# Optimization experiments

Hardware: AMD Instinct MI355X
Metric: run time of the kernel (lower is better)

Reference implementation:

```python
import jax, jax.numpy as jnp
from jax import lax
import numpy as np

BIG = jnp.float32(1e6)  # 'no feature in this column' sentinel distance


def setup_inputs() -> dict:
    key = jax.random.key(0)
    k1, k2 = jax.random.split(key)
    # Binary segmentation masks in {0,1}; surf() only uses astype(bool), i.e. != 0.
    pred = (jax.random.uniform(k1, (512, 512)) > 0.5).astype(jnp.float32)
    gt = (jax.random.uniform(k2, (512, 512)) > 0.5).astype(jnp.float32)
    return {"pred": pred, "gt": gt}


def _erode(x):
    # scipy binary_erosion with connectivity-1 (cross) structure, border_value=0:
    # pixel survives iff it and its 4 neighbors are all True (out-of-bounds = False).
    p = jnp.pad(x, 1, constant_values=False)
    return x & p[:-2, 1:-1] & p[2:, 1:-1] & p[1:-1, :-2] & p[1:-1, 2:]


def _edt(feat):
    # Exact Euclidean distance from every pixel to the nearest True pixel of `feat`.
    # Equals scipy distance_transform_edt(~feat) in the original code.
    H, W = feat.shape
    # --- pass 1: per-column 1D distance |r - k| to nearest feature (two sweeps) ---
    def sweep(carry, row):
        c = jnp.where(row, jnp.float32(0.0), carry + jnp.float32(1.0))
        return c, c
    init = jnp.full((W,), BIG, dtype=jnp.float32)
    _, df = lax.scan(sweep, init, feat)          # distance to nearest feature above
    _, db = lax.scan(sweep, init, feat[::-1])    # ... below
    g = jnp.minimum(df, db[::-1])                # [H, W] vertical distance
    g2 = g * g
    # --- pass 2: row-wise min-plus over column offsets (exact, separable) ---
    j = jnp.arange(W, dtype=jnp.float32)
    delta2 = (j[:, None] - j[None, :]) ** 2      # [W(c), W(j)]
    # D[r, c] = min_j ( g2[r, j] + (c - j)^2 )   -> [H, W, W] intermediate
    d2 = jnp.min(g2[:, None, :] + delta2[None, :, :], axis=-1)
    return jnp.sqrt(d2)


def reference(pred, gt):
    p = pred != 0
    g = gt != 0
    # Surface = mask minus its erosion
    S = p & ~_erode(p)
    Sprime = g & ~_erode(g)
    dta = _edt(S)       # distance field to pred surface (== edt(~S))
    dtb = _edt(Sprime)  # distance field to gt surface
    sm = S.astype(jnp.float32)
    spm = Sprime.astype(jnp.float32)
    # mean of concat(dta[Sprime], dtb[S]) without dynamic shapes
    num = jnp.sum(dta * spm) + jnp.sum(dtb * sm)
    den = jnp.sum(spm) + jnp.sum(sm)
    return num / den
```

## Files before the change

### kernel.cpp

```cpp
#include <hip/hip_runtime.h>

#define HH 512
#define WW 512
#define NB HH

__device__ unsigned int g_ticket = 0;

#define AT_LD(p)    __hip_atomic_load((p),       __ATOMIC_RELAXED, __HIP_MEMORY_SCOPE_AGENT)
#define AT_ST(p, v) __hip_atomic_store((p), (v), __ATOMIC_RELAXED, __HIP_MEMORY_SCOPE_AGENT)
#define AT_ADD(p)   __hip_atomic_fetch_add((p), 1u, __ATOMIC_RELAXED, __HIP_MEMORY_SCOPE_AGENT)

__device__ __forceinline__ unsigned int surf2(const float* __restrict__ pa,
                                              const float* __restrict__ pb,
                                              int ru, int c) {
    const int base = ru * WW + c;
    float a_c = pa[base];
    float b_c = pb[base];
    float a_u = (ru > 0)      ? pa[base - WW] : 0.0f;
    float b_u = (ru > 0)      ? pb[base - WW] : 0.0f;
    float a_d = (ru < HH - 1) ? pa[base + WW] : 0.0f;
    float b_d = (ru < HH - 1) ? pb[base + WW] : 0.0f;
    float a_l = (c > 0)       ? pa[base - 1]  : 0.0f;
    float b_l = (c > 0)       ? pb[base - 1]  : 0.0f;
    float a_r = (c < WW - 1)  ? pa[base + 1]  : 0.0f;
    float b_r = (c < WW - 1)  ? pb[base + 1]  : 0.0f;
    unsigned int bits = 0u;
    if (a_c != 0.0f && !(a_u != 0.0f && a_d != 0.0f && a_l != 0.0f && a_r != 0.0f)) bits |= 1u;
    if (b_c != 0.0f && !(b_u != 0.0f && b_d != 0.0f && b_l != 0.0f && b_r != 0.0f)) bits |= 2u;
    return bits;
}

__global__ __launch_bounds__(512) void fused_kernel(
        const float* __restrict__ pred, const float* __restrict__ gt,
        double* __restrict__ partials, float* __restrict__ out) {
    __shared__ float2 s2[WW];
    __shared__ double lred[16];
    __shared__ int    winner;
    const int r = blockIdx.x;
    const int c = threadIdx.x;

    unsigned int own = surf2(pred, gt, r, c);
    bool fa = (own & 1u) != 0u;
    bool fb = (own & 2u) != 0u;
    int foundA = fa ? 0 : -1;
    int foundB = fb ? 0 : -1;
    for (int k = 1; k < HH && (foundA < 0 || foundB < 0); ++k) {
        int ru = r - k, rd = r + k;
        if (ru < 0 && rd >= HH) break;
        unsigned int hit = 0u;
        if (ru >= 0) hit |= surf2(pred, gt, ru, c);
        if (rd < HH) hit |= surf2(pred, gt, rd, c);
        if (foundA < 0 && (hit & 1u)) foundA = k;
        if (foundB < 0 && (hit & 2u)) foundB = k;
    }
    float sent = 1e6f + (float)((r + 1 < HH - r) ? (r + 1) : (HH - r));
    float ga = (foundA >= 0) ? (float)foundA : sent;
    float gb = (foundB >= 0) ? (float)foundB : sent;
    s2[c] = make_float2(ga * ga, gb * gb);
    __syncthreads();

    float2 o2 = s2[c];
    float besta = o2.x, bestb = o2.y;
    for (int kb = 1; kb < WW; kb += 4) {
        float kk2 = (float)(kb * kb);
        if (kk2 >= besta && kk2 >= bestb) break;
        #pragma unroll
        for (int i = 0; i < 4; ++i) {
            int k = kb + i;
            float k2 = (float)(k * k);
            int cl = c - k, cr = c + k;
            if (cl >= 0) {
                float2 g = s2[cl];
                besta = fminf(besta, g.x + k2);
                bestb = fminf(bestb, g.y + k2);
            }
            if (cr < WW) {
                float2 g = s2[cr];
                besta = fminf(besta, g.x + k2);
                bestb = fminf(bestb, g.y + k2);
            }
        }
    }

    float wA = fa ? 1.0f : 0.0f;
    float wB = fb ? 1.0f : 0.0f;
    double lnum = (double)(sqrtf(besta) * wB + sqrtf(bestb) * wA);
    double lden = (double)(wA + wB);
    for (int off = 32; off > 0; off >>= 1) {
        lnum += __shfl_down(lnum, off, 64);
        lden += __shfl_down(lden, off, 64);
    }
    int wv = c >> 6;
    if ((c & 63) == 0) { lred[wv] = lnum; lred[8 + wv] = lden; }
    __syncthreads();
    if (c == 0) {
        double n = 0.0, d = 0.0;
        #pragma unroll
        for (int i = 0; i < 8; ++i) { n += lred[i]; d += lred[8 + i]; }
        AT_ST(&partials[2 * r],     n);
        AT_ST(&partials[2 * r + 1], d);
        asm volatile("s_waitcnt vmcnt(0) lgkmcnt(0)" ::: "memory");
        unsigned int old = AT_ADD(&g_ticket);
        winner = (old == NB - 1u) ? 1 : 0;
    }
    __syncthreads();

    if (winner) {
        double n = AT_LD(&partials[2 * c]);
        double d = AT_LD(&partials[2 * c + 1]);
        for (int off = 32; off > 0; off >>= 1) {
            n += __shfl_down(n, off, 64);
            d += __shfl_down(d, off, 64);
        }
        if ((c & 63) == 0) { lred[c >> 6] = n; lred[8 + (c >> 6)] = d; }
        __syncthreads();
        if (c == 0) {
            double nn = 0.0, dd = 0.0;
            #pragma unroll
            for (int i = 0; i < 8; ++i) { nn += lred[i]; dd += lred[8 + i]; }
            out[0] = (float)(nn / dd);
            AT_ST(&g_ticket, 0u);
        }
    }
}

extern "C" void kernel_launch(void* const* d_in, const int* in_sizes, int n_in,
                              void* d_out, int out_size, void* d_ws, size_t ws_size,
                              hipStream_t stream) {
    const float* pred = (const float*)d_in[0];
    const float* gt   = (const float*)d_in[1];
    float* out = (float*)d_out;

    double* partials = (double*)d_ws;

    fused_kernel<<<dim3(NB), dim3(WW), 0, stream>>>(pred, gt, partials, out);
}
```

Measured before the change: 79.39 us.

## Stage mask rows in shared memory ring buffers for vertical surface search

```diff
diff --git a/kernel.cpp b/kernel.cpp
--- a/kernel.cpp
+++ b/kernel.cpp
@@ -10,49 +10,69 @@
 #define AT_ST(p, v) __hip_atomic_store((p), (v), __ATOMIC_RELAXED, __HIP_MEMORY_SCOPE_AGENT)
 #define AT_ADD(p)   __hip_atomic_fetch_add((p), 1u, __ATOMIC_RELAXED, __HIP_MEMORY_SCOPE_AGENT)
 
-__device__ __forceinline__ unsigned int surf2(const float* __restrict__ pa,
-                                              const float* __restrict__ pb,
-                                              int ru, int c) {
-    const int base = ru * WW + c;
-    float a_c = pa[base];
-    float b_c = pb[base];
-    float a_u = (ru > 0)      ? pa[base - WW] : 0.0f;
-    float b_u = (ru > 0)      ? pb[base - WW] : 0.0f;
-    float a_d = (ru < HH - 1) ? pa[base + WW] : 0.0f;
-    float b_d = (ru < HH - 1) ? pb[base + WW] : 0.0f;
-    float a_l = (c > 0)       ? pa[base - 1]  : 0.0f;
-    float b_l = (c > 0)       ? pb[base - 1]  : 0.0f;
-    float a_r = (c < WW - 1)  ? pa[base + 1]  : 0.0f;
-    float b_r = (c < WW - 1)  ? pb[base + 1]  : 0.0f;
-    unsigned int bits = 0u;
-    if (a_c != 0.0f && !(a_u != 0.0f && a_d != 0.0f && a_l != 0.0f && a_r != 0.0f)) bits |= 1u;
-    if (b_c != 0.0f && !(b_u != 0.0f && b_d != 0.0f && b_l != 0.0f && b_r != 0.0f)) bits |= 2u;
-    return bits;
-}
-
 __global__ __launch_bounds__(512) void fused_kernel(
         const float* __restrict__ pred, const float* __restrict__ gt,
         double* __restrict__ partials, float* __restrict__ out) {
+    __shared__ unsigned int uR[3][WW + 2];
+    __shared__ unsigned int dR[3][WW + 2];
     __shared__ float2 s2[WW];
     __shared__ double lred[16];
     __shared__ int    winner;
     const int r = blockIdx.x;
     const int c = threadIdx.x;
 
-    unsigned int own = surf2(pred, gt, r, c);
+    if (c < 6) {
+        int s = c >> 1;
+        int p = (c & 1) ? (WW + 1) : 0;
+        uR[s][p] = 0u;
+        dR[s][p] = 0u;
+    }
+
+    auto mbits = [&](int row) -> unsigned int {
+        unsigned int b = 0u;
+        if (row >= 0 && row < HH) {
+            if (pred[row * WW + c] != 0.0f) b |= 1u;
+            if (gt[row * WW + c]   != 0.0f) b |= 2u;
+        }
+        return b;
+    };
+
+    unsigned int b0 = mbits(r);
+    uR[0][c + 1] = b0;
+    dR[0][c + 1] = b0;
+    uR[1][c + 1] = mbits(r - 1);
+    dR[1][c + 1] = mbits(r + 1);
+    __syncthreads();
+
+    unsigned int own = uR[0][c + 1] &
+        ~(uR[1][c + 1] & dR[1][c + 1] & uR[0][c] & uR[0][c + 2]);
     bool fa = (own & 1u) != 0u;
     bool fb = (own & 2u) != 0u;
     int foundA = fa ? 0 : -1;
     int foundB = fb ? 0 : -1;
-    for (int k = 1; k < HH && (foundA < 0 || foundB < 0); ++k) {
-        int ru = r - k, rd = r + k;
-        if (ru < 0 && rd >= HH) break;
+    bool done = (foundA >= 0) && (foundB >= 0);
+
+    for (int k = 1; k < HH; ++k) {
+        if (__syncthreads_and((int)done)) break;
+        const int sl = (k + 1) % 3;
+        uR[sl][c + 1] = mbits(r - k - 1);
+        dR[sl][c + 1] = mbits(r + k + 1);
+        __syncthreads();
         unsigned int hit = 0u;
-        if (ru >= 0) hit |= surf2(pred, gt, ru, c);
-        if (rd < HH) hit |= surf2(pred, gt, rd, c);
+        const int km = k % 3, kp = (k - 1 + 3) % 3;
+        if (r - k >= 0) {
+            hit |= uR[km][c + 1] &
+                ~(uR[sl][c + 1] & uR[kp][c + 1] & uR[km][c] & uR[km][c + 2]);
+        }
+        if (r + k < HH) {
+            hit |= dR[km][c + 1] &
+                ~(dR[sl][c + 1] & dR[kp][c + 1] & dR[km][c] & dR[km][c + 2]);
+        }
         if (foundA < 0 && (hit & 1u)) foundA = k;
         if (foundB < 0 && (hit & 2u)) foundB = k;
+        done = (foundA >= 0) && (foundB >= 0);
     }
+
     float sent = 1e6f + (float)((r + 1 < HH - r) ? (r + 1) : (HH - r));
     float ga = (foundA >= 0) ? (float)foundA : sent;
     float gb = (foundB >= 0) ? (float)foundB : sent;
```

After: 70.81 us. 1.12x faster.
